# Optimization experiments

Measured on AMD Instinct MI355X. Metric: run time of the kernel, lower is better.

The kernel has to match this reference:

```python
import jax, jax.numpy as jnp
import numpy as np

C = 256      # in/out channels
PSI = 4
W = C // PSI          # window width = 64
D = W // 2            # stride = 32
HEADS = 2 * PSI - 1   # 7


def conv_bn_relu(x, Wmat, scale, bias):
    # 1x1 conv (no bias) + inference-mode BN (folded to per-channel scale/bias) + ReLU
    y = jnp.einsum('oc,bcn->bon', Wmat, x)
    return jax.nn.relu(y * scale[:, None] + bias[:, None])


def setup_inputs() -> dict:
    key = jax.random.key(0)
    ks = jax.random.split(key, 16)
    B, N = 4, 2048
    x = jax.random.normal(ks[0], (B, C, N), dtype=jnp.float32)
    Wq = jax.random.normal(ks[1], (C, C), dtype=jnp.float32) / np.sqrt(C)
    Wk = jax.random.normal(ks[2], (C, C), dtype=jnp.float32) / np.sqrt(C)
    Wv = jax.random.normal(ks[3], (C, C), dtype=jnp.float32) / np.sqrt(C)
    sq = jax.random.uniform(ks[4], (C,), dtype=jnp.float32, minval=0.5, maxval=1.5)
    bq = jax.random.normal(ks[5], (C,), dtype=jnp.float32) * 0.1
    sk = jax.random.uniform(ks[6], (C,), dtype=jnp.float32, minval=0.5, maxval=1.5)
    bk = jax.random.normal(ks[7], (C,), dtype=jnp.float32) * 0.1
    sv = jax.random.uniform(ks[8], (C,), dtype=jnp.float32, minval=0.5, maxval=1.5)
    bv = jax.random.normal(ks[9], (C,), dtype=jnp.float32) * 0.1
    Wf = jax.random.normal(ks[10], (C, HEADS * W), dtype=jnp.float32) / np.sqrt(HEADS * W)
    bf = jax.random.normal(ks[11], (C,), dtype=jnp.float32) * 0.1
    sf = jax.random.uniform(ks[12], (C,), dtype=jnp.float32, minval=0.5, maxval=1.5)
    bff = jax.random.normal(ks[13], (C,), dtype=jnp.float32) * 0.1
    return dict(x=x, Wq=Wq, sq=sq, bq=bq, Wk=Wk, sk=sk, bk=bk,
                Wv=Wv, sv=sv, bv=bv, Wf=Wf, bf=bf, sf=sf, bff=bff)


def reference(x, Wq, sq, bq, Wk, sk, bk, Wv, sv, bv, Wf, bf, sf, bff):
    q = conv_bn_relu(x, Wq, sq, bq)   # [B, C, N]
    k = conv_bn_relu(x, Wk, sk, bk)
    v = conv_bn_relu(x, Wv, sv, bv)

    # overlapping channel windows: head m covers channels [m*D, m*D+W)
    win = jnp.arange(HEADS)[:, None] * D + jnp.arange(W)[None, :]  # [HEADS, W]
    qw = q[:, win, :]  # [B, HEADS, W, N]
    kw = k[:, win, :]
    vw = v[:, win, :]

    # a_m = q_m^T k_m over channel window -> [B, HEADS, N, N]
    attn = jnp.einsum('bhwn,bhwm->bhnm', qw, kw)
    attn = jax.nn.softmax(attn, axis=-1)
    # o_m = (a_m v_m^T)^T -> [B, HEADS, W, N]
    o = jnp.einsum('bhnm,bhwm->bhwn', attn, vw)

    B, _, _, N = o.shape
    O = o.reshape(B, HEADS * W, N)  # concat heads along channel dim

    # fusion: 1x1 conv (with bias) + BN + ReLU
    y = jnp.einsum('oc,bcn->bon', Wf, O) + bf[:, None]
    return jax.nn.relu(y * sf[:, None] + bff[:, None])
```

## Files before the change

### kernel.cpp

```cpp
#include <hip/hip_runtime.h>
#include <hip/hip_bf16.h>

typedef __attribute__((ext_vector_type(8))) short bf16x8;
typedef __attribute__((ext_vector_type(4))) float f32x4;

namespace {
constexpr int kC = 256;
constexpr int kN = 2048;
constexpr int kB = 4;
constexpr int kHeads = 7;
constexpr int kOC = kHeads * 64;
constexpr int kSplit = 2;
constexpr int kMChunk = kN / kSplit;
constexpr float kLog2e = 1.44269504f;
}

static __device__ __forceinline__ float bf2f(ushort u) {
    union { unsigned u; float f; } v; v.u = ((unsigned)u) << 16;
    return v.f;
}
static __device__ __forceinline__ unsigned pk_bf16(float a, float b) {
    __hip_bfloat162 h = __float22bfloat162_rn(make_float2(a, b));
    union { __hip_bfloat162 h; unsigned u; } v; v.h = h;
    return v.u;
}
static __device__ __forceinline__ ushort4 pack4bf(float a, float b, float c, float d) {
    union { ushort4 s; uint2 u; } v;
    v.u.x = pk_bf16(a, b); v.u.y = pk_bf16(c, d);
    return v.s;
}
static __device__ __forceinline__ float fexp2(float x) {
#if __has_builtin(__builtin_amdgcn_exp2f)
    return __builtin_amdgcn_exp2f(x);
#else
    return exp2f(x);
#endif
}
static __device__ __forceinline__ void g2l16(const ushort* g, ushort* l) {
    __builtin_amdgcn_global_load_lds(
        (const __attribute__((address_space(1))) void*)g,
        (__attribute__((address_space(3))) void*)l,
        16, 0, 0);
}

__global__ __launch_bounds__(256) void cast_w_kernel(
    const float* __restrict__ Wq, const float* __restrict__ Wk,
    const float* __restrict__ Wv, const float* __restrict__ Wf,
    ushort* __restrict__ wq, ushort* __restrict__ wk,
    ushort* __restrict__ wv, ushort* __restrict__ wf)
{
    int which = blockIdx.y;
    const float* src = which == 0 ? Wq : which == 1 ? Wk : which == 2 ? Wv : Wf;
    ushort* dst      = which == 0 ? wq : which == 1 ? wk : which == 2 ? wv : wf;
    int n = (which == 3) ? kC * kOC : kC * kC;
    int i = (blockIdx.x * 256 + threadIdx.x) * 4;
    if (i < n) {
        float4 v = *(const float4*)(src + i);
        *(ushort4*)(dst + i) = pack4bf(v.x, v.y, v.z, v.w);
    }
}

__global__ __launch_bounds__(256) void transpose_kernel(
    const float* __restrict__ x, ushort* __restrict__ xT)
{
    const int nt = blockIdx.x, ct = blockIdx.y, b = blockIdx.z;
    __shared__ float T[64][65];
    const int tid = threadIdx.x;
    const float* xb = x + ((size_t)b * kC + ct * 64) * kN + nt * 64;
#pragma unroll
    for (int p = 0; p < 16; ++p) {
        int idx = p * 256 + tid;
        int cc = idx >> 6, nn = idx & 63;
        T[cc][nn] = xb[(size_t)cc * kN + nn];
    }
    __syncthreads();
    ushort* xTb = xT + ((size_t)b * kN + nt * 64) * kC + ct * 64;
#pragma unroll
    for (int p = 0; p < 4; ++p) {
        int nn = p * 16 + (tid >> 4);
        int c4 = (tid & 15) * 4;
        *(ushort4*)&xTb[(size_t)nn * kC + c4] =
            pack4bf(T[c4 + 0][nn], T[c4 + 1][nn], T[c4 + 2][nn], T[c4 + 3][nn]);
    }
}

__global__ __launch_bounds__(256, 2) void qkv_kernel(
    const ushort* __restrict__ xT,
    const ushort* __restrict__ Wqb, const ushort* __restrict__ Wkb, const ushort* __restrict__ Wvb,
    const float* __restrict__ sq, const float* __restrict__ bq,
    const float* __restrict__ sk, const float* __restrict__ bk,
    const float* __restrict__ sv, const float* __restrict__ bv,
    ushort* __restrict__ qT, ushort* __restrict__ kT, ushort* __restrict__ vB)
{
    const int nt  = blockIdx.x;
    const int ot  = blockIdx.y;
    const int b   = blockIdx.z / 3;
    const int mat = blockIdx.z % 3;
    const ushort* Wb = mat == 0 ? Wqb : mat == 1 ? Wkb : Wvb;
    const float* sm = mat == 0 ? sq : mat == 1 ? sk : sv;
    const float* bm = mat == 0 ? bq : mat == 1 ? bk : bv;

    __shared__ __align__(16) ushort lds[4][128 * 64];

    const int tid = threadIdx.x;
    const int lane = tid & 63, wav = tid >> 6;
    const int quad = lane >> 4, l16 = lane & 15;

    const ushort* xTb = xT + ((size_t)b * kN + nt * 128) * kC;
    const ushort* Wt  = Wb + (size_t)(ot * 128) * kC;

    f32x4 acc[8][2];
#pragma unroll
    for (int mt = 0; mt < 8; ++mt)
#pragma unroll
        for (int ntt = 0; ntt < 2; ++ntt)
#pragma unroll
            for (int r = 0; r < 4; ++r) acc[mt][ntt][r] = 0.f;

    const int sa   = lane >> 3;
    const int sblk = (lane & 7) ^ sa;
    auto dmaK = [&](int k0, int buf) {
#pragma unroll
        for (int p = 0; p < 4; ++p) {
            int row = wav * 32 + p * 8 + sa;
            size_t so = (size_t)row * kC + k0 + sblk * 8;
            int dbase = (wav * 32 + p * 8) * 64;
            g2l16(Wt + so,  &lds[buf][dbase]);
            g2l16(xTb + so, &lds[2 + buf][dbase]);
        }
    };

    dmaK(0, 0);
    __syncthreads();

    for (int kt = 0; kt < 4; ++kt) {
        const int cur = kt & 1;
        const bool more = (kt < 3);
        if (more) dmaK((kt + 1) * 64, cur ^ 1);

        const ushort* rowB = (mat < 2) ? lds[cur] : lds[2 + cur];
        const ushort* colB = (mat < 2) ? lds[2 + cur] : lds[cur];
#pragma unroll
        for (int ks = 0; ks < 2; ++ks) {
            bf16x8 bfr[2];
#pragma unroll
            for (int ntt = 0; ntt < 2; ++ntt) {
                int row = wav * 32 + ntt * 16 + l16;
                bfr[ntt] = *(const bf16x8*)&colB[row * 64 + (((ks * 4 + quad) ^ (row & 7)) * 8)];
            }
#pragma unroll
            for (int mt = 0; mt < 8; ++mt) {
                int row = mt * 16 + l16;
                bf16x8 af = *(const bf16x8*)&rowB[row * 64 + (((ks * 4 + quad) ^ (row & 7)) * 8)];
#pragma unroll
                for (int ntt = 0; ntt < 2; ++ntt)
                    acc[mt][ntt] = __builtin_amdgcn_mfma_f32_16x16x32_bf16(
                        af, bfr[ntt], acc[mt][ntt], 0, 0, 0);
            }
        }
        __syncthreads();
    }

    ushort* sT = &lds[0][0];
    const float qs = (mat == 0) ? kLog2e : 1.f;

    if (mat < 2) {
#pragma unroll
        for (int mt = 0; mt < 8; ++mt) {
            float4 sc4 = *(const float4*)&sm[ot * 128 + mt * 16 + quad * 4];
            float4 bi4 = *(const float4*)&bm[ot * 128 + mt * 16 + quad * 4];
#pragma unroll
            for (int ntt = 0; ntt < 2; ++ntt) {
                int nrow = wav * 32 + ntt * 16 + l16;
                float v0 = fmaf(acc[mt][ntt][0], sc4.x, bi4.x) * qs;
                float v1 = fmaf(acc[mt][ntt][1], sc4.y, bi4.y) * qs;
                float v2 = fmaf(acc[mt][ntt][2], sc4.z, bi4.z) * qs;
                float v3 = fmaf(acc[mt][ntt][3], sc4.w, bi4.w) * qs;
                int cb = (mt * 2 + (quad >> 1)) ^ (nrow & 15);
                *(ushort4*)&sT[nrow * 128 + cb * 8 + (quad & 1) * 4] =
                    pack4bf(v0 > 0.f ? v0 : 0.f, v1 > 0.f ? v1 : 0.f,
                            v2 > 0.f ? v2 : 0.f, v3 > 0.f ? v3 : 0.f);
            }
        }
        __syncthreads();
        ushort* out = (mat == 0) ? qT : kT;
#pragma unroll
        for (int p = 0; p < 8; ++p) {
            int idx = p * 256 + tid;
            int row = idx >> 4, blk = idx & 15;
            int4 d = *(const int4*)&sT[row * 128 + ((blk ^ (row & 15)) * 8)];
            *(int4*)&out[((size_t)b * kN + nt * 128 + row) * kC + ot * 128 + blk * 8] = d;
        }
    } else {
#pragma unroll
        for (int ntt = 0; ntt < 2; ++ntt) {
            int orow = wav * 32 + ntt * 16 + l16;
            float sc = sm[ot * 128 + orow], bi = bm[ot * 128 + orow];
#pragma unroll
            for (int mt = 0; mt < 8; ++mt) {
                float v0 = fmaf(acc[mt][ntt][0], sc, bi);
                float v1 = fmaf(acc[mt][ntt][1], sc, bi);
                float v2 = fmaf(acc[mt][ntt][2], sc, bi);
                float v3 = fmaf(acc[mt][ntt][3], sc, bi);
                int cb = (mt * 2 + (quad >> 1)) ^ (orow & 15);
                *(ushort4*)&sT[orow * 128 + cb * 8 + (quad & 1) * 4] =
                    pack4bf(v0 > 0.f ? v0 : 0.f, v1 > 0.f ? v1 : 0.f,
                            v2 > 0.f ? v2 : 0.f, v3 > 0.f ? v3 : 0.f);
            }
        }
        __syncthreads();
#pragma unroll
        for (int p = 0; p < 8; ++p) {
            int idx = p * 256 + tid;
            int row = idx >> 4, blk = idx & 15;
            int4 d = *(const int4*)&sT[row * 128 + ((blk ^ (row & 15)) * 8)];
            *(int4*)&vB[((size_t)b * kC + ot * 128 + row) * kN + nt * 128 + blk * 8] = d;
        }
    }
}

__global__ __launch_bounds__(256, 3) void attn_kernel(
    const ushort* __restrict__ qT, const ushort* __restrict__ kT,
    const ushort* __restrict__ vB,
    ushort* __restrict__ Opart, float* __restrict__ Ls)
{
    const int n0 = blockIdx.x * 128;
    const int h  = blockIdx.y;
    const int s  = blockIdx.z & 1;
    const int b  = blockIdx.z >> 1;
    const int tid = threadIdx.x;
    const int lane = tid & 63, wav = tid >> 6;
    const int quad = lane >> 4, l16 = lane & 15;

    __shared__ __align__(16) ushort sKV[2][8192];
    __shared__ __align__(16) ushort sP[128 * 64];

    const ushort* qTb = qT + (size_t)b * kN * kC;
    const ushort* kTb = kT + (size_t)b * kN * kC;
    const ushort* vbb = vB + ((size_t)b * kC + h * 32) * kN;

    const int arr   = wav >> 1;
    const int rbase = (wav & 1) * 32;

    bf16x8 qf[2][2];
#pragma unroll
    for (int kk = 0; kk < 2; ++kk)
#pragma unroll
        for (int nt2 = 0; nt2 < 2; ++nt2) {
            int ng = n0 + wav * 32 + nt2 * 16 + l16;
            qf[kk][nt2] = *(const bf16x8*)(qTb + (size_t)ng * kC + h * 32 + kk * 32 + quad * 8);
        }

    f32x4 oacc[4][2];
#pragma unroll
    for (int wt = 0; wt < 4; ++wt)
#pragma unroll
        for (int nt2 = 0; nt2 < 2; ++nt2)
#pragma unroll
            for (int r = 0; r < 4; ++r) oacc[wt][nt2][r] = 0.f;
    float li[2] = {0.f, 0.f};

    const int mstart = s * kMChunk;
    const int NIT = kMChunk / 64;

    const int sa   = lane >> 3;
    const int sblk = (lane & 7) ^ sa;
    auto dmaTile = [&](int m0, int buf) {
#pragma unroll
        for (int p = 0; p < 4; ++p) {
            int rl = rbase + p * 8 + sa;
            const ushort* src = (arr == 0)
                ? (kTb + (size_t)(m0 + rl) * kC + h * 32 + sblk * 8)
                : (vbb + (size_t)rl * kN + m0 + sblk * 8);
            g2l16(src, &sKV[buf][arr * 4096 + (rbase + p * 8) * 64]);
        }
    };

    dmaTile(mstart, 0);
    __syncthreads();

    for (int it = 0; it < NIT; ++it) {
        const int cur = it & 1;
        const bool more = (it + 1 < NIT);
        if (more) dmaTile(mstart + (it + 1) * 64, cur ^ 1);

        const ushort* sK = &sKV[cur][0];
        const ushort* sV = &sKV[cur][4096];

        f32x4 sacc[4][2];
#pragma unroll
        for (int mt = 0; mt < 4; ++mt)
#pragma unroll
            for (int nt2 = 0; nt2 < 2; ++nt2)
#pragma unroll
                for (int r = 0; r < 4; ++r) sacc[mt][nt2][r] = 0.f;
#pragma unroll
        for (int kk = 0; kk < 2; ++kk)
#pragma unroll
            for (int mt = 0; mt < 4; ++mt) {
                int row = mt * 16 + l16;
                bf16x8 af = *(const bf16x8*)&sK[row * 64 + (((kk * 4 + quad) ^ (row & 7)) * 8)];
#pragma unroll
                for (int nt2 = 0; nt2 < 2; ++nt2)
                    sacc[mt][nt2] = __builtin_amdgcn_mfma_f32_16x16x32_bf16(
                        af, qf[kk][nt2], sacc[mt][nt2], 0, 0, 0);
            }

#pragma unroll
        for (int nt2 = 0; nt2 < 2; ++nt2) {
            int nrow = wav * 32 + nt2 * 16 + l16;
            float sum = 0.f;
#pragma unroll
            for (int mt = 0; mt < 4; ++mt) {
                float p0 = fexp2(sacc[mt][nt2][0]);
                float p1 = fexp2(sacc[mt][nt2][1]);
                float p2 = fexp2(sacc[mt][nt2][2]);
                float p3 = fexp2(sacc[mt][nt2][3]);
                sum += (p0 + p1) + (p2 + p3);
                int bidx = (mt * 2 + (quad >> 1)) ^ (nrow & 7);
                uint2 pk; pk.x = pk_bf16(p0, p1); pk.y = pk_bf16(p2, p3);
                *(uint2*)&sP[nrow * 64 + bidx * 8 + (quad & 1) * 4] = pk;
            }
            sum += __shfl_xor(sum, 16);
            sum += __shfl_xor(sum, 32);
            li[nt2] += sum;
        }

#pragma unroll
        for (int ks = 0; ks < 2; ++ks) {
            bf16x8 pf[2];
#pragma unroll
            for (int nt2 = 0; nt2 < 2; ++nt2) {
                int nr = wav * 32 + nt2 * 16 + l16;
                pf[nt2] = *(const bf16x8*)&sP[nr * 64 + (((ks * 4 + quad) ^ (nr & 7)) * 8)];
            }
#pragma unroll
            for (int wt = 0; wt < 4; ++wt) {
                int wr = wt * 16 + l16;
                bf16x8 vf = *(const bf16x8*)&sV[wr * 64 + (((ks * 4 + quad) ^ (wr & 7)) * 8)];
#pragma unroll
                for (int nt2 = 0; nt2 < 2; ++nt2)
                    oacc[wt][nt2] = __builtin_amdgcn_mfma_f32_16x16x32_bf16(
                        vf, pf[nt2], oacc[wt][nt2], 0, 0, 0);
            }
        }

        __syncthreads();
    }

#pragma unroll
    for (int nt2 = 0; nt2 < 2; ++nt2) {
        if (quad == 0) {
            int n = n0 + wav * 32 + nt2 * 16 + l16;
            size_t si = ((size_t)(s * kB + b) * kHeads + h) * kN + n;
            Ls[si] = li[nt2];
        }
    }
    ushort* sT = sP;
#pragma unroll
    for (int wt = 0; wt < 4; ++wt)
#pragma unroll
        for (int nt2 = 0; nt2 < 2; ++nt2) {
            float inv = 1.f / li[nt2];
            int nrow = wav * 32 + nt2 * 16 + l16;
            int cb = (wt * 2 + (quad >> 1)) ^ (nrow & 7);
            *(ushort4*)&sT[nrow * 64 + cb * 8 + (quad & 1) * 4] =
                pack4bf(oacc[wt][nt2][0] * inv, oacc[wt][nt2][1] * inv,
                        oacc[wt][nt2][2] * inv, oacc[wt][nt2][3] * inv);
        }
    __syncthreads();
    int rsub = tid >> 3, blk = tid & 7;
#pragma unroll
    for (int p = 0; p < 4; ++p) {
        int row = p * 32 + rsub;
        int4 d = *(const int4*)&sT[row * 64 + ((blk ^ (row & 7)) * 8)];
        *(int4*)&Opart[((size_t)s * kB * kN + (size_t)b * kN + n0 + row) * kOC
                       + h * 64 + blk * 8] = d;
    }
}

__global__ __launch_bounds__(128, 3) void proj_kernel(
    const ushort* __restrict__ Opart, const float* __restrict__ Ls,
    const ushort* __restrict__ Wfb,
    const float* __restrict__ bf_, const float* __restrict__ sf,
    const float* __restrict__ bff, float* __restrict__ out)
{
    const int nt = blockIdx.x;
    const int ot = blockIdx.y;
    const int b  = blockIdx.z;
    __shared__ __align__(16) ushort sA[2][64 * 64];
    __shared__ __align__(16) ushort sB[2][64 * 64];
    const int tid = threadIdx.x;
    const int lane = tid & 63, wav = tid >> 6;
    const int quad = lane >> 4, l16 = lane & 15;

    const ushort* Wt  = Wfb + (size_t)(ot * 64) * kOC;
    const ushort* Op1 = Opart;
    const ushort* Op2 = Opart + (size_t)kB * kN * kOC;
    const size_t soff = (size_t)kB * kHeads * kN;

    f32x4 acc[4][2];
#pragma unroll
    for (int mt = 0; mt < 4; ++mt)
#pragma unroll
        for (int ntt = 0; ntt < 2; ++ntt)
#pragma unroll
            for (int r = 0; r < 4; ++r) acc[mt][ntt][r] = 0.f;

    int4 areg[4], b1reg[4], b2reg[4];
    float w1a[4], w2a[4];

    auto prefetch = [&](int kt) {
        int k0 = kt * 64;
#pragma unroll
        for (int p = 0; p < 4; ++p) {
            int idx = p * 128 + tid, row = idx >> 3, blk = idx & 7;
            areg[p] = *(const int4*)(Wt + (size_t)row * kOC + k0 + blk * 8);
            int n = nt * 64 + row;
            size_t bo = ((size_t)b * kN + n) * kOC + k0 + blk * 8;
            b1reg[p] = *(const int4*)(Op1 + bo);
            b2reg[p] = *(const int4*)(Op2 + bo);
            size_t si = ((size_t)b * kHeads + kt) * kN + n;
            float l1 = Ls[si], l2 = Ls[si + soff];
            float inv = 1.f / (l1 + l2);
            w1a[p] = l1 * inv; w2a[p] = l2 * inv;
        }
    };
    auto stage = [&](int buf) {
#pragma unroll
        for (int p = 0; p < 4; ++p) {
            int idx = p * 128 + tid, row = idx >> 3, blk = idx & 7;
            *(int4*)&sA[buf][row * 64 + ((blk ^ (row & 7)) * 8)] = areg[p];
            union { int4 v; ushort u[8]; } a, c;
            a.v = b1reg[p]; c.v = b2reg[p];
            float rr[8];
#pragma unroll
            for (int j = 0; j < 8; ++j)
                rr[j] = bf2f(a.u[j]) * w1a[p] + bf2f(c.u[j]) * w2a[p];
            int4 o;
            o.x = (int)pk_bf16(rr[0], rr[1]);
            o.y = (int)pk_bf16(rr[2], rr[3]);
            o.z = (int)pk_bf16(rr[4], rr[5]);
            o.w = (int)pk_bf16(rr[6], rr[7]);
            *(int4*)&sB[buf][row * 64 + ((blk ^ (row & 7)) * 8)] = o;
        }
    };

    prefetch(0);
    stage(0);
    __syncthreads();

    for (int kt = 0; kt < 7; ++kt) {
        const int cur = kt & 1;
        const bool more = (kt < 6);
        if (more) prefetch(kt + 1);
#pragma unroll
        for (int ks = 0; ks < 2; ++ks) {
            bf16x8 bfr[2];
#pragma unroll
            for (int ntt = 0; ntt < 2; ++ntt) {
                int row = wav * 32 + ntt * 16 + l16;
                bfr[ntt] = *(const bf16x8*)&sB[cur][row * 64 + (((ks * 4 + quad) ^ (row & 7)) * 8)];
            }
#pragma unroll
            for (int mt = 0; mt < 4; ++mt) {
                int row = mt * 16 + l16;
                bf16x8 af = *(const bf16x8*)&sA[cur][row * 64 + (((ks * 4 + quad) ^ (row & 7)) * 8)];
#pragma unroll
                for (int ntt = 0; ntt < 2; ++ntt)
                    acc[mt][ntt] = __builtin_amdgcn_mfma_f32_16x16x32_bf16(
                        af, bfr[ntt], acc[mt][ntt], 0, 0, 0);
            }
        }
        if (more) stage(cur ^ 1);
        __syncthreads();
    }
#pragma unroll
    for (int mt = 0; mt < 4; ++mt)
#pragma unroll
        for (int r = 0; r < 4; ++r) {
            int o = ot * 64 + mt * 16 + quad * 4 + r;
            float bfv = bf_[o], sfv = sf[o], bffv = bff[o];
#pragma unroll
            for (int ntt = 0; ntt < 2; ++ntt) {
                int n = nt * 64 + wav * 32 + ntt * 16 + l16;
                float y = fmaf(acc[mt][ntt][r] + bfv, sfv, bffv);
                out[((size_t)b * kC + o) * kN + n] = y > 0.f ? y : 0.f;
            }
        }
}

extern "C" void kernel_launch(void* const* d_in, const int* in_sizes, int n_in,
                              void* d_out, int out_size, void* d_ws, size_t ws_size,
                              hipStream_t stream) {
    const float* x   = (const float*)d_in[0];
    const float* Wq  = (const float*)d_in[1];
    const float* sq  = (const float*)d_in[2];
    const float* bq  = (const float*)d_in[3];
    const float* Wk  = (const float*)d_in[4];
    const float* sk  = (const float*)d_in[5];
    const float* bk  = (const float*)d_in[6];
    const float* Wv  = (const float*)d_in[7];
    const float* sv  = (const float*)d_in[8];
    const float* bv  = (const float*)d_in[9];
    const float* Wf  = (const float*)d_in[10];
    const float* bf_ = (const float*)d_in[11];
    const float* sf  = (const float*)d_in[12];
    const float* bff = (const float*)d_in[13];
    float* out = (float*)d_out;

    char* ws = (char*)d_ws;
    ushort* xT  = (ushort*)(ws);
    ushort* Wqb = (ushort*)(ws + 4194304);
    ushort* Wkb = (ushort*)(ws + 4325376);
    ushort* Wvb = (ushort*)(ws + 4456448);
    ushort* Wfb = (ushort*)(ws + 4587520);
    ushort* qT  = (ushort*)(ws + 4816896);
    ushort* kT  = (ushort*)(ws + 9011200);
    ushort* vB  = (ushort*)(ws + 13205504);
    ushort* Opart = (ushort*)(ws + 17399808);
    float*  Ls  = (float*)(ws + 32079872);

    cast_w_kernel<<<dim3(112, 4), 256, 0, stream>>>(Wq, Wk, Wv, Wf, Wqb, Wkb, Wvb, Wfb);
    transpose_kernel<<<dim3(kN / 64, kC / 64, kB), 256, 0, stream>>>(x, xT);
    qkv_kernel<<<dim3(kN / 128, kC / 128, kB * 3), 256, 0, stream>>>(
        xT, Wqb, Wkb, Wvb, sq, bq, sk, bk, sv, bv, qT, kT, vB);
    attn_kernel<<<dim3(kN / 128, kHeads, kB * kSplit), 256, 0, stream>>>(
        qT, kT, vB, Opart, Ls);
    proj_kernel<<<dim3(kN / 64, kC / 64, kB), 128, 0, stream>>>(
        Opart, Ls, Wfb, bf_, sf, bff, out);
}
```

Before: 166.0 us.

## Pass softmax P through register shuffles and widen proj kernel to four waves

The attention kernel now builds the bf16 P operand for the PV MFMA with cross-lane shuffles instead of writing it to shared memory and reading it back. This frees the separate sP buffer, so LDS use per block drops and the occupancy hint rises from 3 to 4. The projection kernel moves from 128 to 256 threads, each wave owning a 16-row output slice across four column tiles, with halved prefetch registers. In exchange the attention loop does extra shuffle and select work, and the proj kernel issues more LDS reads per MFMA.

```diff
diff --git a/kernel.cpp b/kernel.cpp
--- a/kernel.cpp
+++ b/kernel.cpp
@@ -219,7 +219,7 @@
     }
 }
 
-__global__ __launch_bounds__(256, 3) void attn_kernel(
+__global__ __launch_bounds__(256, 4) void attn_kernel(
     const ushort* __restrict__ qT, const ushort* __restrict__ kT,
     const ushort* __restrict__ vB,
     ushort* __restrict__ Opart, float* __restrict__ Ls)
@@ -233,7 +233,6 @@
     const int quad = lane >> 4, l16 = lane & 15;
 
     __shared__ __align__(16) ushort sKV[2][8192];
-    __shared__ __align__(16) ushort sP[128 * 64];
 
     const ushort* qTb = qT + (size_t)b * kN * kC;
     const ushort* kTb = kT + (size_t)b * kN * kC;
@@ -241,6 +240,10 @@
 
     const int arr   = wav >> 1;
     const int rbase = (wav & 1) * 32;
+
+    const int gx = ((lane & 16) << 1) + l16;
+    const int gy = gx + 16;
+    const bool lo = (lane < 32);
 
     bf16x8 qf[2][2];
 #pragma unroll
@@ -306,9 +309,9 @@
                         af, qf[kk][nt2], sacc[mt][nt2], 0, 0, 0);
             }
 
+        unsigned d[2][4][2];
 #pragma unroll
         for (int nt2 = 0; nt2 < 2; ++nt2) {
-            int nrow = wav * 32 + nt2 * 16 + l16;
             float sum = 0.f;
 #pragma unroll
             for (int mt = 0; mt < 4; ++mt) {
@@ -317,9 +320,8 @@
                 float p2 = fexp2(sacc[mt][nt2][2]);
                 float p3 = fexp2(sacc[mt][nt2][3]);
                 sum += (p0 + p1) + (p2 + p3);
-                int bidx = (mt * 2 + (quad >> 1)) ^ (nrow & 7);
-                uint2 pk; pk.x = pk_bf16(p0, p1); pk.y = pk_bf16(p2, p3);
-                *(uint2*)&sP[nrow * 64 + bidx * 8 + (quad & 1) * 4] = pk;
+                d[nt2][mt][0] = pk_bf16(p0, p1);
+                d[nt2][mt][1] = pk_bf16(p2, p3);
             }
             sum += __shfl_xor(sum, 16);
             sum += __shfl_xor(sum, 32);
@@ -331,8 +333,18 @@
             bf16x8 pf[2];
 #pragma unroll
             for (int nt2 = 0; nt2 < 2; ++nt2) {
-                int nr = wav * 32 + nt2 * 16 + l16;
-                pf[nt2] = *(const bf16x8*)&sP[nr * 64 + (((ks * 4 + quad) ^ (nr & 7)) * 8)];
+                union { unsigned w[4]; bf16x8 v8; } pu;
+#pragma unroll
+                for (int rd = 0; rd < 2; ++rd) {
+                    unsigned u = d[nt2][2 * ks][rd], v = d[nt2][2 * ks + 1][rd];
+                    unsigned xu = (unsigned)__shfl((int)u, gx);
+                    unsigned xv = (unsigned)__shfl((int)v, gx);
+                    unsigned yu = (unsigned)__shfl((int)u, gy);
+                    unsigned yv = (unsigned)__shfl((int)v, gy);
+                    pu.w[rd]     = lo ? xu : xv;
+                    pu.w[2 + rd] = lo ? yu : yv;
+                }
+                pf[nt2] = pu.v8;
             }
 #pragma unroll
             for (int wt = 0; wt < 4; ++wt) {
@@ -356,7 +368,7 @@
             Ls[si] = li[nt2];
         }
     }
-    ushort* sT = sP;
+    ushort* sT = &sKV[0][0];
 #pragma unroll
     for (int wt = 0; wt < 4; ++wt)
 #pragma unroll
@@ -373,13 +385,13 @@
 #pragma unroll
     for (int p = 0; p < 4; ++p) {
         int row = p * 32 + rsub;
-        int4 d = *(const int4*)&sT[row * 64 + ((blk ^ (row & 7)) * 8)];
+        int4 dd = *(const int4*)&sT[row * 64 + ((blk ^ (row & 7)) * 8)];
         *(int4*)&Opart[((size_t)s * kB * kN + (size_t)b * kN + n0 + row) * kOC
-                       + h * 64 + blk * 8] = d;
-    }
-}
-
-__global__ __launch_bounds__(128, 3) void proj_kernel(
+                       + h * 64 + blk * 8] = dd;
+    }
+}
+
+__global__ __launch_bounds__(256, 4) void proj_kernel(
     const ushort* __restrict__ Opart, const float* __restrict__ Ls,
     const ushort* __restrict__ Wfb,
     const float* __restrict__ bf_, const float* __restrict__ sf,
@@ -399,22 +411,20 @@
     const ushort* Op2 = Opart + (size_t)kB * kN * kOC;
     const size_t soff = (size_t)kB * kHeads * kN;
 
-    f32x4 acc[4][2];
-#pragma unroll
-    for (int mt = 0; mt < 4; ++mt)
-#pragma unroll
-        for (int ntt = 0; ntt < 2; ++ntt)
-#pragma unroll
-            for (int r = 0; r < 4; ++r) acc[mt][ntt][r] = 0.f;
-
-    int4 areg[4], b1reg[4], b2reg[4];
-    float w1a[4], w2a[4];
+    f32x4 acc[4];
+#pragma unroll
+    for (int ntt = 0; ntt < 4; ++ntt)
+#pragma unroll
+        for (int r = 0; r < 4; ++r) acc[ntt][r] = 0.f;
+
+    int4 areg[2], b1reg[2], b2reg[2];
+    float w1a[2], w2a[2];
 
     auto prefetch = [&](int kt) {
         int k0 = kt * 64;
 #pragma unroll
-        for (int p = 0; p < 4; ++p) {
-            int idx = p * 128 + tid, row = idx >> 3, blk = idx & 7;
+        for (int p = 0; p < 2; ++p) {
+            int idx = p * 256 + tid, row = idx >> 3, blk = idx & 7;
             areg[p] = *(const int4*)(Wt + (size_t)row * kOC + k0 + blk * 8);
             int n = nt * 64 + row;
             size_t bo = ((size_t)b * kN + n) * kOC + k0 + blk * 8;
@@ -428,8 +438,8 @@
     };
     auto stage = [&](int buf) {
 #pragma unroll
-        for (int p = 0; p < 4; ++p) {
-            int idx = p * 128 + tid, row = idx >> 3, blk = idx & 7;
+        for (int p = 0; p < 2; ++p) {
+            int idx = p * 256 + tid, row = idx >> 3, blk = idx & 7;
             *(int4*)&sA[buf][row * 64 + ((blk ^ (row & 7)) * 8)] = areg[p];
             union { int4 v; ushort u[8]; } a, c;
             a.v = b1reg[p]; c.v = b2reg[p];
@@ -456,38 +466,29 @@
         if (more) prefetch(kt + 1);
 #pragma unroll
         for (int ks = 0; ks < 2; ++ks) {
-            bf16x8 bfr[2];
-#pragma unroll
-            for (int ntt = 0; ntt < 2; ++ntt) {
-                int row = wav * 32 + ntt * 16 + l16;
-                bfr[ntt] = *(const bf16x8*)&sB[cur][row * 64 + (((ks * 4 + quad) ^ (row & 7)) * 8)];
-            }
-#pragma unroll
-            for (int mt = 0; mt < 4; ++mt) {
-                int row = mt * 16 + l16;
-                bf16x8 af = *(const bf16x8*)&sA[cur][row * 64 + (((ks * 4 + quad) ^ (row & 7)) * 8)];
-#pragma unroll
-                for (int ntt = 0; ntt < 2; ++ntt)
-                    acc[mt][ntt] = __builtin_amdgcn_mfma_f32_16x16x32_bf16(
-                        af, bfr[ntt], acc[mt][ntt], 0, 0, 0);
+            int arow = wav * 16 + l16;
+            bf16x8 af = *(const bf16x8*)&sA[cur][arow * 64 + (((ks * 4 + quad) ^ (arow & 7)) * 8)];
+#pragma unroll
+            for (int ntt = 0; ntt < 4; ++ntt) {
+                int brow = ntt * 16 + l16;
+                bf16x8 bfr = *(const bf16x8*)&sB[cur][brow * 64 + (((ks * 4 + quad) ^ (brow & 7)) * 8)];
+                acc[ntt] = __builtin_amdgcn_mfma_f32_16x16x32_bf16(af, bfr, acc[ntt], 0, 0, 0);
             }
         }
         if (more) stage(cur ^ 1);
         __syncthreads();
     }
 #pragma unroll
-    for (int mt = 0; mt < 4; ++mt)
-#pragma unroll
-        for (int r = 0; r < 4; ++r) {
-            int o = ot * 64 + mt * 16 + quad * 4 + r;
-            float bfv = bf_[o], sfv = sf[o], bffv = bff[o];
-#pragma unroll
-            for (int ntt = 0; ntt < 2; ++ntt) {
-                int n = nt * 64 + wav * 32 + ntt * 16 + l16;
-                float y = fmaf(acc[mt][ntt][r] + bfv, sfv, bffv);
-                out[((size_t)b * kC + o) * kN + n] = y > 0.f ? y : 0.f;
-            }
-        }
+    for (int r = 0; r < 4; ++r) {
+        int o = ot * 64 + wav * 16 + quad * 4 + r;
+        float bfv = bf_[o], sfv = sf[o], bffv = bff[o];
+#pragma unroll
+        for (int ntt = 0; ntt < 4; ++ntt) {
+            int n = nt * 64 + ntt * 16 + l16;
+            float y = fmaf(acc[ntt][r] + bfv, sfv, bffv);
+            out[((size_t)b * kC + o) * kN + n] = y > 0.f ? y : 0.f;
+        }
+    }
 }
 
 extern "C" void kernel_launch(void* const* d_in, const int* in_sizes, int n_in,
@@ -527,6 +528,6 @@
         xT, Wqb, Wkb, Wvb, sq, bq, sk, bk, sv, bv, qT, kT, vB);
     attn_kernel<<<dim3(kN / 128, kHeads, kB * kSplit), 256, 0, stream>>>(
         qT, kT, vB, Opart, Ls);
-    proj_kernel<<<dim3(kN / 64, kC / 64, kB), 128, 0, stream>>>(
+    proj_kernel<<<dim3(kN / 64, kC / 64, kB), 256, 0, stream>>>(
         Opart, Ls, Wfb, bf_, sf, bff, out);
 }
```

New measurement: 168.1 us. No clear change (+1.2%).
